# Performance work log

Measured on AMD Instinct MI355X. Metric: run time of the kernel, lower is better.

The kernel has to match this reference:

```python
import jax, jax.numpy as jnp
from jax import lax
import numpy as np

WINDOW_SIZE = 11
SIGMA = 1.5  # create_windows hardcodes 1.5, ignoring self.sigma
C1 = 0.01 ** 2
C2 = 0.03 ** 2


def _gaussian(ws, sigma):
    x = np.arange(ws, dtype=np.float32)
    g = np.exp(-((x - ws // 2) ** 2) / (2.0 * sigma ** 2))
    return (g / g.sum()).astype(np.float32)


def _blur(x, window):
    # Separable depthwise Gaussian blur with 'same' symmetric padding.
    # x: [N, 1, H, W]; window: [ws]
    ws = window.shape[0]
    p = ws // 2
    dn = ('NCHW', 'OIHW', 'NCHW')
    kh = window.reshape(1, 1, ws, 1)
    kw = window.reshape(1, 1, 1, ws)
    x = lax.conv_general_dilated(x, kh, (1, 1), [(p, p), (0, 0)], dimension_numbers=dn)
    x = lax.conv_general_dilated(x, kw, (1, 1), [(0, 0), (p, p)], dimension_numbers=dn)
    return x


def setup_inputs() -> dict:
    key = jax.random.key(0)
    k1, k2 = jax.random.split(key)
    shape = (16, 1, 1024, 1024)
    img1 = jax.random.uniform(k1, shape, dtype=jnp.float32)
    img2 = jax.random.uniform(k2, shape, dtype=jnp.float32)
    window = jnp.asarray(_gaussian(WINDOW_SIZE, SIGMA))
    return {"img1": img1, "img2": img2, "window": window}


def reference(img1, img2, window):
    mu1 = _blur(img1, window)
    mu2 = _blur(img2, window)
    mu1_sq = mu1 * mu1
    mu2_sq = mu2 * mu2
    mu1_mu2 = mu1 * mu2
    sigma1_sq = _blur(img1 * img1, window) - mu1_sq
    sigma2_sq = _blur(img2 * img2, window) - mu2_sq
    sigma12 = _blur(img1 * img2, window) - mu1_mu2
    ssim_map = ((2.0 * mu1_mu2 + C1) * (2.0 * sigma12 + C2)) / (
        (mu1_sq + mu2_sq + C1) * (sigma1_sq + sigma2_sq + C2))
    return jnp.mean(ssim_map)  # size_average=True
```

## Files before the change

### kernel.cpp

```cpp
#include <hip/hip_runtime.h>


typedef float f4 __attribute__((ext_vector_type(4)));

#define W      1024
#define H      1024
#define NIMG   16
#define HALO   5
#define BX     128
#define OUTW   118
#define RPS    8
#define NSTG   4
#define TH     (RPS*NSTG)
#define GX     9
#define GY     (H/TH)
#define NBLK   (GX*GY*NIMG)

__device__ __forceinline__ int swz(int s) { return s ^ ((s >> 3) & 7); }

template<bool INT>
__device__ __forceinline__ void pf_row(const float* __restrict__ p1,
                                       const float* __restrict__ p2,
                                       int j, int c, bool cOK,
                                       float& a, float& b)
{
    if (INT) {
        a = p1[(size_t)j * W + c];
        b = p2[(size_t)j * W + c];
    } else {
        const bool ok = cOK && ((unsigned)j < H);
        a = ok ? p1[(size_t)j * W + c] : 0.0f;
        b = ok ? p2[(size_t)j * W + c] : 0.0f;
    }
}

__device__ __forceinline__ f4 pack_ch(float a, float b)
{
    f4 v;
    v.x = a; v.y = b;
    v.z = fmaf(a, a, b * b);
    v.w = a * b;
    return v;
}

__device__ __forceinline__ void vstage_reg(const float* __restrict__ w,
                                           const float (&pa)[RPS], const float (&pb)[RPS],
                                           f4 (&ring)[11], f4 (*buf)[BX], int ws_)
{
#pragma unroll
    for (int rr = 0; rr < RPS; ++rr) {
#pragma unroll
        for (int k = 0; k < 10; ++k) ring[k] = ring[k + 1];
        ring[10] = pack_ch(pa[rr], pb[rr]);

        f4 acc = w[5] * ring[5];
#pragma unroll
        for (int k = 0; k < 5; ++k)
            acc += w[k] * (ring[k] + ring[10 - k]);

        buf[rr][ws_] = acc;
    }
}

template<bool INT>
__device__ float tile(const float* __restrict__ p1,
                      const float* __restrict__ p2,
                      const float* __restrict__ w,
                      int cb, int r0, int t,
                      f4 (*lds)[BX])
{
    const int  c   = cb + t;
    const bool cOK = INT || ((unsigned)c < W);

    f4 ring[11];
#pragma unroll
    for (int k = 0; k < 10; ++k) {
        float a, b;
        pf_row<INT>(p1, p2, r0 - HALO + k, c, cOK, a, b);
        ring[k + 1] = pack_ch(a, b);
    }

    const int  q   = t >> 4;
    const int  run = t & 15;
    const int  S0  = 8 * run;
    const bool hT  = (run < 15);
    const int  ws_ = swz(t);

    float pa[RPS], pb[RPS];

#pragma unroll
    for (int rr = 0; rr < RPS; ++rr)
        pf_row<INT>(p1, p2, r0 + HALO + rr, c, cOK, pa[rr], pb[rr]);
    vstage_reg(w, pa, pb, ring, lds, ws_);
    __syncthreads();

    float tsum = 0.0f;

    for (int st = 0; st < NSTG; ++st) {
        if (st + 1 < NSTG) {
#pragma unroll
            for (int rr = 0; rr < RPS; ++rr)
                pf_row<INT>(p1, p2, r0 + (st + 1) * RPS + HALO + rr, c, cOK,
                            pa[rr], pb[rr]);
        }

        if (hT) {
            f4 o[8] = {};
#pragma unroll
            for (int i = 0; i < 18; ++i) {
                int sIdx = S0 + i;
                sIdx = (sIdx < BX) ? sIdx : (BX - 1);
                const f4 u = lds[q][swz(sIdx)];
#pragma unroll
                for (int oo = 0; oo < 8; ++oo) {
                    const int k = i - oo;
                    if (k >= 0 && k < 11)
                        o[oo] += w[k] * u;
                }
            }

            const float C1f = 0.0001f, C2f = 0.0009f;
#pragma unroll
            for (int oo = 0; oo < 8; ++oo) {
                const int rel = S0 + oo;
                const bool valid = (rel < OUTW) &&
                                   (INT || (cb + HALO + rel) < W);
                if (valid) {
                    const float m1 = o[oo].x, m2 = o[oo].y;
                    const float qq = o[oo].z, pp = o[oo].w;
                    const float mu12 = m1 * m2, m1s = m1 * m1, m2s = m2 * m2;
                    const float s12 = pp - mu12;
                    const float ssq = qq - m1s - m2s;
                    const float num = (2.f * mu12 + C1f) * (2.f * s12 + C2f);
                    const float den = (m1s + m2s + C1f) * (ssq + C2f);
                    tsum += num * __builtin_amdgcn_rcpf(den);
                }
            }
        }
        __syncthreads();

        if (st + 1 < NSTG) {
            vstage_reg(w, pa, pb, ring, lds, ws_);
            __syncthreads();
        }
    }
    return tsum;
}

__global__ __launch_bounds__(BX) void ssim_main(const float* __restrict__ img1,
                                                const float* __restrict__ img2,
                                                const float* __restrict__ win,
                                                float* __restrict__ partials)
{
    __shared__ f4 lds[RPS][BX];

    const int t  = threadIdx.x;
    const int n  = blockIdx.z;
    const int bx = blockIdx.x;
    const int gy = blockIdx.y;
    const int cb = bx * OUTW - HALO;
    const int r0 = gy * TH;

    const float* __restrict__ p1 = img1 + (size_t)n * (size_t)(W * H);
    const float* __restrict__ p2 = img2 + (size_t)n * (size_t)(W * H);

    float w[11];
#pragma unroll
    for (int k = 0; k < 11; ++k)
        w[k] = __int_as_float(__builtin_amdgcn_readfirstlane(__float_as_int(win[k])));

    const bool interior = (cb >= 0) && (cb + BX <= W) &&
                          (r0 >= HALO) && (r0 + TH - 1 + HALO < H);

    float tsum = interior ? tile<true >(p1, p2, w, cb, r0, t, lds)
                          : tile<false>(p1, p2, w, cb, r0, t, lds);

#pragma unroll
    for (int off = 32; off > 0; off >>= 1)
        tsum += __shfl_down(tsum, off, 64);

    float* red = (float*)lds;
    if ((t & 63) == 0) red[t >> 6] = tsum;
    __syncthreads();
    if (t == 0)
        partials[((size_t)n * GY + gy) * GX + bx] = red[0] + red[1];
}

__global__ __launch_bounds__(256) void ssim_finalize(const float* __restrict__ partials,
                                                     float* __restrict__ out)
{
    double s = 0.0;
    for (int i = threadIdx.x; i < NBLK; i += 256) s += (double)partials[i];
#pragma unroll
    for (int off = 32; off > 0; off >>= 1)
        s += __shfl_down(s, off, 64);

    __shared__ double ws[4];
    if ((threadIdx.x & 63) == 0) ws[threadIdx.x >> 6] = s;
    __syncthreads();
    if (threadIdx.x == 0) {
        const double tt = ws[0] + ws[1] + ws[2] + ws[3];
        out[0] = (float)(tt / (double)((size_t)NIMG * W * H));
    }
}

extern "C" void kernel_launch(void* const* d_in, const int* in_sizes, int n_in,
                              void* d_out, int out_size, void* d_ws, size_t ws_size,
                              hipStream_t stream)
{
    const float* img1 = (const float*)d_in[0];
    const float* img2 = (const float*)d_in[1];
    const float* win  = (const float*)d_in[2];
    float* partials   = (float*)d_ws;
    float* out        = (float*)d_out;

    dim3 grid(GX, GY, NIMG);
    dim3 block(BX);
    ssim_main<<<grid, block, 0, stream>>>(img1, img2, win, partials);
    ssim_finalize<<<1, 256, 0, stream>>>(partials, out);
}
```

Measured before the change: 62.18 us.

## Split tiles into independent per-wave 64-column strips without block barriers

Each 64-lane wave now owns its own 64-wide column strip (54 outputs) and its own LDS slab, computing the vertical and horizontal passes with no __syncthreads. Work is indexed by a flat wave id, with per-wave partial sums and taller tiles (8 stages). This removes block-level barrier stalls and lets waves run out of sync with each other. In exchange, halo overhead roughly doubles, with more redundant global loads and vertical work per output, and correctness relies on wave-synchronous LDS ordering.

```diff
diff --git a/kernel.cpp b/kernel.cpp
--- a/kernel.cpp
+++ b/kernel.cpp
@@ -7,16 +7,17 @@
 #define H      1024
 #define NIMG   16
 #define HALO   5
-#define BX     128
-#define OUTW   118
+#define TW     64
+#define TOW    54
 #define RPS    8
-#define NSTG   4
+#define NSTG   8
 #define TH     (RPS*NSTG)
-#define GX     9
-#define GY     (H/TH)
-#define NBLK   (GX*GY*NIMG)
-
-__device__ __forceinline__ int swz(int s) { return s ^ ((s >> 3) & 7); }
+#define NTX    19
+#define NTY    (H/TH)
+#define WPB    4
+#define BX     (WPB*64)
+#define NWAVE  (NTX*NTY*NIMG)
+#define NBLK   (NWAVE/WPB)
 
 template<bool INT>
 __device__ __forceinline__ void pf_row(const float* __restrict__ p1,
@@ -43,33 +44,14 @@
     return v;
 }
 
-__device__ __forceinline__ void vstage_reg(const float* __restrict__ w,
-                                           const float (&pa)[RPS], const float (&pb)[RPS],
-                                           f4 (&ring)[11], f4 (*buf)[BX], int ws_)
-{
-#pragma unroll
-    for (int rr = 0; rr < RPS; ++rr) {
-#pragma unroll
-        for (int k = 0; k < 10; ++k) ring[k] = ring[k + 1];
-        ring[10] = pack_ch(pa[rr], pb[rr]);
-
-        f4 acc = w[5] * ring[5];
-#pragma unroll
-        for (int k = 0; k < 5; ++k)
-            acc += w[k] * (ring[k] + ring[10 - k]);
-
-        buf[rr][ws_] = acc;
-    }
-}
-
 template<bool INT>
-__device__ float tile(const float* __restrict__ p1,
-                      const float* __restrict__ p2,
-                      const float* __restrict__ w,
-                      int cb, int r0, int t,
-                      f4 (*lds)[BX])
-{
-    const int  c   = cb + t;
+__device__ float wave_tile(const float* __restrict__ p1,
+                           const float* __restrict__ p2,
+                           const float* __restrict__ w,
+                           int cb, int r0, int lane, int obase,
+                           f4 (*lds)[TW])
+{
+    const int  c   = cb + lane;
     const bool cOK = INT || ((unsigned)c < W);
 
     f4 ring[11];
@@ -80,23 +62,32 @@
         ring[k + 1] = pack_ch(a, b);
     }
 
-    const int  q   = t >> 4;
-    const int  run = t & 15;
-    const int  S0  = 8 * run;
-    const bool hT  = (run < 15);
-    const int  ws_ = swz(t);
+    const int q   = lane >> 3;
+    const int run = lane & 7;
+    const int S0  = 7 * run;
 
     float pa[RPS], pb[RPS];
-
 #pragma unroll
     for (int rr = 0; rr < RPS; ++rr)
         pf_row<INT>(p1, p2, r0 + HALO + rr, c, cOK, pa[rr], pb[rr]);
-    vstage_reg(w, pa, pb, ring, lds, ws_);
-    __syncthreads();
 
     float tsum = 0.0f;
 
     for (int st = 0; st < NSTG; ++st) {
+#pragma unroll
+        for (int rr = 0; rr < RPS; ++rr) {
+#pragma unroll
+            for (int k = 0; k < 10; ++k) ring[k] = ring[k + 1];
+            ring[10] = pack_ch(pa[rr], pb[rr]);
+
+            f4 acc = w[5] * ring[5];
+#pragma unroll
+            for (int k = 0; k < 5; ++k)
+                acc += w[k] * (ring[k] + ring[10 - k]);
+
+            lds[rr][lane] = acc;
+        }
+
         if (st + 1 < NSTG) {
 #pragma unroll
             for (int rr = 0; rr < RPS; ++rr)
@@ -104,15 +95,15 @@
                             pa[rr], pb[rr]);
         }
 
-        if (hT) {
-            f4 o[8] = {};
-#pragma unroll
-            for (int i = 0; i < 18; ++i) {
-                int sIdx = S0 + i;
-                sIdx = (sIdx < BX) ? sIdx : (BX - 1);
-                const f4 u = lds[q][swz(sIdx)];
-#pragma unroll
-                for (int oo = 0; oo < 8; ++oo) {
+        {
+            f4 o[7] = {};
+#pragma unroll
+            for (int i = 0; i < 17; ++i) {
+                int s = S0 + i;
+                s = (s < TW) ? s : (TW - 1);
+                const f4 u = lds[q][s];
+#pragma unroll
+                for (int oo = 0; oo < 7; ++oo) {
                     const int k = i - oo;
                     if (k >= 0 && k < 11)
                         o[oo] += w[k] * u;
@@ -121,10 +112,9 @@
 
             const float C1f = 0.0001f, C2f = 0.0009f;
 #pragma unroll
-            for (int oo = 0; oo < 8; ++oo) {
+            for (int oo = 0; oo < 7; ++oo) {
                 const int rel = S0 + oo;
-                const bool valid = (rel < OUTW) &&
-                                   (INT || (cb + HALO + rel) < W);
+                const bool valid = (rel < TOW) && (INT || (obase + rel) < W);
                 if (valid) {
                     const float m1 = o[oo].x, m2 = o[oo].y;
                     const float qq = o[oo].z, pp = o[oo].w;
@@ -137,12 +127,6 @@
                 }
             }
         }
-        __syncthreads();
-
-        if (st + 1 < NSTG) {
-            vstage_reg(w, pa, pb, ring, lds, ws_);
-            __syncthreads();
-        }
     }
     return tsum;
 }
@@ -152,45 +136,50 @@
                                                 const float* __restrict__ win,
                                                 float* __restrict__ partials)
 {
-    __shared__ f4 lds[RPS][BX];
-
-    const int t  = threadIdx.x;
-    const int n  = blockIdx.z;
-    const int bx = blockIdx.x;
-    const int gy = blockIdx.y;
-    const int cb = bx * OUTW - HALO;
-    const int r0 = gy * TH;
-
-    const float* __restrict__ p1 = img1 + (size_t)n * (size_t)(W * H);
-    const float* __restrict__ p2 = img2 + (size_t)n * (size_t)(W * H);
+    __shared__ f4 lds[WPB][RPS][TW];
+
+    const int t    = threadIdx.x;
+    const int wid  = t >> 6;
+    const int lane = t & 63;
+    const int gw   = blockIdx.x * WPB + wid;
+
+    const int img = gw / (NTX * NTY);
+    const int rem = gw - img * (NTX * NTY);
+    const int gy  = rem / NTX;
+    const int tx  = rem - gy * NTX;
+
+    const int cb    = tx * TOW - HALO;
+    const int obase = tx * TOW;
+    const int r0    = gy * TH;
+
+    const float* __restrict__ p1 = img1 + (size_t)img * (size_t)(W * H);
+    const float* __restrict__ p2 = img2 + (size_t)img * (size_t)(W * H);
 
     float w[11];
 #pragma unroll
     for (int k = 0; k < 11; ++k)
         w[k] = __int_as_float(__builtin_amdgcn_readfirstlane(__float_as_int(win[k])));
 
-    const bool interior = (cb >= 0) && (cb + BX <= W) &&
+    const bool interior = (cb >= 0) && (cb + TW <= W) &&
                           (r0 >= HALO) && (r0 + TH - 1 + HALO < H);
 
-    float tsum = interior ? tile<true >(p1, p2, w, cb, r0, t, lds)
-                          : tile<false>(p1, p2, w, cb, r0, t, lds);
+    float tsum = interior
+               ? wave_tile<true >(p1, p2, w, cb, r0, lane, obase, lds[wid])
+               : wave_tile<false>(p1, p2, w, cb, r0, lane, obase, lds[wid]);
 
 #pragma unroll
     for (int off = 32; off > 0; off >>= 1)
         tsum += __shfl_down(tsum, off, 64);
 
-    float* red = (float*)lds;
-    if ((t & 63) == 0) red[t >> 6] = tsum;
-    __syncthreads();
-    if (t == 0)
-        partials[((size_t)n * GY + gy) * GX + bx] = red[0] + red[1];
+    if (lane == 0)
+        partials[gw] = tsum;
 }
 
 __global__ __launch_bounds__(256) void ssim_finalize(const float* __restrict__ partials,
                                                      float* __restrict__ out)
 {
     double s = 0.0;
-    for (int i = threadIdx.x; i < NBLK; i += 256) s += (double)partials[i];
+    for (int i = threadIdx.x; i < NWAVE; i += 256) s += (double)partials[i];
 #pragma unroll
     for (int off = 32; off > 0; off >>= 1)
         s += __shfl_down(s, off, 64);
@@ -214,8 +203,6 @@
     float* partials   = (float*)d_ws;
     float* out        = (float*)d_out;
 
-    dim3 grid(GX, GY, NIMG);
-    dim3 block(BX);
-    ssim_main<<<grid, block, 0, stream>>>(img1, img2, win, partials);
+    ssim_main<<<NBLK, BX, 0, stream>>>(img1, img2, win, partials);
     ssim_finalize<<<1, 256, 0, stream>>>(partials, out);
 }
```

Measured after the change: 61.06 us. No clear change (-1.8%).
